# Performance work log

Hardware: AMD Instinct MI355X
Metric: run time of the kernel (lower is better)

## Reference

```python
import jax, jax.numpy as jnp
import numpy as np

B, S = 32, 256          # batch, sequence
D = 128                 # d_model
I = 256                 # mamba intermediate = 2*D
N = 16                  # ssm state size
R = 8                   # dt rank = ceil(D/16)
K = 4                   # conv kernel
L = 4                   # num mamba layers
Z = 128                 # vib z_dim
FUT = 20                # future steps


def setup_inputs() -> dict:
    key = jax.random.key(0)
    ks = iter(jax.random.split(key, 40))

    def nrm(shape, scale=0.02):
        return jax.random.normal(next(ks), shape, dtype=jnp.float32) * scale

    return {
        "x_cam": jax.random.normal(next(ks), (B, S, 8, 1024), dtype=jnp.float32),
        "x_ego": jax.random.normal(next(ks), (B, S, 64), dtype=jnp.float32),
        "vib_eps": jax.random.normal(next(ks), (B, Z), dtype=jnp.float32),
        "vis_w1": nrm((8 * 1024, 512)), "vis_b1": jnp.zeros((512,), jnp.float32),
        "vis_w2": nrm((512, D)), "vis_b2": jnp.zeros((D,), jnp.float32),
        "ego_w": nrm((64, D)), "ego_b": jnp.zeros((D,), jnp.float32),
        "fus_w": nrm((2 * D, D)), "fus_b": jnp.zeros((D,), jnp.float32),
        "norm_w": jnp.ones((L, D), jnp.float32),
        "in_proj_w": nrm((L, D, 2 * I)),
        "conv_w": nrm((L, I, K), 0.1), "conv_b": jnp.zeros((L, I), jnp.float32),
        "x_proj_w": nrm((L, I, R + 2 * N)),
        "dt_proj_w": nrm((L, R, I), 0.1), "dt_proj_b": jnp.full((L, I), -2.0, jnp.float32),
        "A_log": jnp.tile(jnp.log(jnp.arange(1, N + 1, dtype=jnp.float32))[None, None, :], (L, I, 1)),
        "D_par": jnp.ones((L, I), jnp.float32),
        "out_proj_w": nrm((L, I, D)),
        "normf_w": jnp.ones((D,), jnp.float32),
        "mu_w": nrm((D, Z)), "mu_b": jnp.zeros((Z,), jnp.float32),
        "lv_w": nrm((D, Z)), "lv_b": jnp.zeros((Z,), jnp.float32),
        "h1_w": nrm((Z, 256)), "h1_b": jnp.zeros((256,), jnp.float32),
        "h2_w": nrm((256, FUT * 2)), "h2_b": jnp.zeros((FUT * 2,), jnp.float32),
    }


def _rms(x, w, eps=1e-5):
    return x * jax.lax.rsqrt(jnp.mean(x * x, axis=-1, keepdims=True) + eps) * w


def _mixer(x, inw, cw, cb, xpw, dtw, dtb, alog, dpar, outw):
    # x: [B,S,D]
    Bb, Ss, _ = x.shape
    h, gate = jnp.split(x @ inw, 2, axis=-1)            # [B,S,I] each
    # depthwise causal conv (kernel K)
    hp = jnp.pad(h, ((0, 0), (K - 1, 0), (0, 0)))
    h = sum(hp[:, k:k + Ss, :] * cw[:, k] for k in range(K)) + cb
    h = jax.nn.silu(h)
    ssm = h @ xpw                                        # [B,S,R+2N]
    dt = jax.nn.softplus(ssm[..., :R] @ dtw + dtb)       # [B,S,I]
    Bm = ssm[..., R:R + N]                               # [B,S,N]
    Cm = ssm[..., R + N:]                                # [B,S,N]
    A = -jnp.exp(alog)                                   # [I,N]
    dA = jnp.exp(dt[..., None] * A)                      # [B,S,I,N]
    dBu = dt[..., None] * Bm[:, :, None, :] * h[..., None]  # [B,S,I,N]

    def step(carry, t):
        dA_t, dBu_t, C_t = t
        carry = carry * dA_t + dBu_t                     # [B,I,N]
        return carry, jnp.einsum('bin,bn->bi', carry, C_t)

    h0 = jnp.zeros((Bb, I, N), dtype=x.dtype)
    _, ys = jax.lax.scan(step, h0, (dA.swapaxes(0, 1), dBu.swapaxes(0, 1), Cm.swapaxes(0, 1)))
    y = ys.swapaxes(0, 1) + h * dpar                     # [B,S,I]
    y = y * jax.nn.silu(gate)
    return y @ outw                                      # [B,S,D]


def _mamba(x, norm_w, in_proj_w, conv_w, conv_b, x_proj_w, dt_proj_w, dt_proj_b, A_log, D_par, out_proj_w, normf_w):
    for l in range(L):
        x = x + _mixer(_rms(x, norm_w[l]), in_proj_w[l], conv_w[l], conv_b[l],
                       x_proj_w[l], dt_proj_w[l], dt_proj_b[l], A_log[l], D_par[l], out_proj_w[l])
    return _rms(x, normf_w)


def _forward(x_cam, x_ego, vib_eps, vis_w1, vis_b1, vis_w2, vis_b2, ego_w, ego_b, fus_w, fus_b,
             norm_w, in_proj_w, conv_w, conv_b, x_proj_w, dt_proj_w, dt_proj_b, A_log, D_par,
             out_proj_w, normf_w, mu_w, mu_b, lv_w, lv_b, h1_w, h1_b, h2_w, h2_b):
    Bb, Ss = x_cam.shape[:2]
    v = x_cam.reshape(Bb, Ss, -1)                                          # [B,S,8192]
    v = jax.nn.gelu(v @ vis_w1 + vis_b1, approximate=False) @ vis_w2 + vis_b2
    e = x_ego @ ego_w + ego_b
    fused = jax.nn.gelu(jnp.concatenate([v, e], axis=-1) @ fus_w + fus_b, approximate=False)
    h = _mamba(fused, norm_w, in_proj_w, conv_w, conv_b, x_proj_w,
               dt_proj_w, dt_proj_b, A_log, D_par, out_proj_w, normf_w)
    last = h[:, -1, :]                                                     # [B,D]
    mu = last @ mu_w + mu_b
    logvar = last @ lv_w + lv_b
    z = mu + vib_eps * jnp.exp(0.5 * logvar)
    kl = -0.5 * jnp.mean(1.0 + logvar - mu * mu - jnp.exp(logvar))
    out = jax.nn.relu(z @ h1_w + h1_b) @ h2_w + h2_b
    return out.reshape(Bb, FUT, 2), kl


def reference(x_cam, x_ego, vib_eps, vis_w1, vis_b1, vis_w2, vis_b2, ego_w, ego_b, fus_w, fus_b,
              norm_w, in_proj_w, conv_w, conv_b, x_proj_w, dt_proj_w, dt_proj_b, A_log, D_par,
              out_proj_w, normf_w, mu_w, mu_b, lv_w, lv_b, h1_w, h1_b, h2_w, h2_b):
    return _forward(x_cam, x_ego, vib_eps, vis_w1, vis_b1, vis_w2, vis_b2, ego_w, ego_b, fus_w, fus_b,
                    norm_w, in_proj_w, conv_w, conv_b, x_proj_w, dt_proj_w, dt_proj_b, A_log, D_par,
                    out_proj_w, normf_w, mu_w, mu_b, lv_w, lv_b, h1_w, h1_b, h2_w, h2_b)
```

## Files before the change

kernel.cpp:

```cpp
#include <hip/hip_runtime.h>
#include <hip/hip_bf16.h>
#include <math.h>

#define BQ 32
#define SQ 256
#define MTOK 8192
#define DD 128
#define II 256
#define NNs 16
#define RRs 8
#define KKs 4
#define LLs 4
#define ZZs 128
#define FUTs 20

typedef __attribute__((ext_vector_type(8))) short bf8v;
typedef __attribute__((ext_vector_type(4))) float f4v;

__device__ __forceinline__ float geluf(float x){ return 0.5f*x*(1.0f+erff(x*0.70710678118654752f)); }
__device__ __forceinline__ float siluf(float x){ return x/(1.0f+__expf(-x)); }
__device__ __forceinline__ float softplusf(float x){ return fmaxf(x,0.0f)+log1pf(__expf(-fabsf(x))); }
__device__ __forceinline__ unsigned short f2bf(float x){
    __hip_bfloat16 h = __float2bfloat16(x);
    return *reinterpret_cast<unsigned short*>(&h);
}

template<int ACT,int ADD,int OUTBF,typename AT>
__launch_bounds__(256,2)
__global__ void gemm_bf16_kernel(const AT* __restrict__ A,
                                 const unsigned short* __restrict__ Bt,
                                 const float* __restrict__ bias,
                                 void* __restrict__ Cv,
                                 int M, int N, int Kd, int ldc)
{
    constexpr int LDK = 72;
    __shared__ unsigned short As[128*LDK];
    __shared__ unsigned short Bs[64*LDK];
    const int tid = threadIdx.x;
    const int w = tid >> 6, lane = tid & 63;
    const int ml = lane & 15, quad = lane >> 4;
    const int rowBase = blockIdx.x * 128, colBase = blockIdx.y * 64;

    f4v acc[2][4];
    #pragma unroll
    for (int i=0;i<2;i++)
      #pragma unroll
      for (int j=0;j<4;j++) acc[i][j] = (f4v){0.f,0.f,0.f,0.f};

    bf8v pa[4], pb[2];
    const int ar = tid >> 3, as8 = (tid & 7) * 8;

    auto loadTile = [&](int kt){
        #pragma unroll
        for (int e=0;e<4;e++){
            int r = ar + e*32;
            if constexpr (sizeof(AT)==2){
                pa[e] = *reinterpret_cast<const bf8v*>(
                    (const unsigned short*)A + (size_t)(rowBase+r)*Kd + kt + as8);
            } else {
                const float* ap = (const float*)A + (size_t)(rowBase+r)*Kd + kt + as8;
                float4 v0 = *reinterpret_cast<const float4*>(ap);
                float4 v1 = *reinterpret_cast<const float4*>(ap+4);
                union { unsigned short u[8]; bf8v v; } o;
                o.u[0]=f2bf(v0.x); o.u[1]=f2bf(v0.y); o.u[2]=f2bf(v0.z); o.u[3]=f2bf(v0.w);
                o.u[4]=f2bf(v1.x); o.u[5]=f2bf(v1.y); o.u[6]=f2bf(v1.z); o.u[7]=f2bf(v1.w);
                pa[e] = o.v;
            }
        }
        #pragma unroll
        for (int e=0;e<2;e++){
            int r = ar + e*32;
            pb[e] = *reinterpret_cast<const bf8v*>(
                Bt + (size_t)(colBase+r)*Kd + kt + as8);
        }
    };

    loadTile(0);

    for (int kt=0; kt<Kd; kt+=64){
        #pragma unroll
        for (int e=0;e<4;e++) *reinterpret_cast<bf8v*>(&As[(ar+e*32)*LDK + as8]) = pa[e];
        #pragma unroll
        for (int e=0;e<2;e++) *reinterpret_cast<bf8v*>(&Bs[(ar+e*32)*LDK + as8]) = pb[e];
        __syncthreads();
        if (kt + 64 < Kd) loadTile(kt + 64);
        #pragma unroll
        for (int ks=0; ks<2; ks++){
            bf8v a0 = *reinterpret_cast<bf8v*>(&As[(w*32 +      ml)*LDK + ks*32 + quad*8]);
            bf8v a1 = *reinterpret_cast<bf8v*>(&As[(w*32 + 16 + ml)*LDK + ks*32 + quad*8]);
            #pragma unroll
            for (int nt=0; nt<4; nt++){
                bf8v b = *reinterpret_cast<bf8v*>(&Bs[(nt*16+ml)*LDK + ks*32 + quad*8]);
                acc[0][nt] = __builtin_amdgcn_mfma_f32_16x16x32_bf16(a0, b, acc[0][nt], 0,0,0);
                acc[1][nt] = __builtin_amdgcn_mfma_f32_16x16x32_bf16(a1, b, acc[1][nt], 0,0,0);
            }
        }
        __syncthreads();
    }

    #pragma unroll
    for (int mt=0; mt<2; mt++){
        #pragma unroll
        for (int nt=0; nt<4; nt++){
            int col = colBase + nt*16 + ml;
            float bb = bias ? bias[col] : 0.0f;
            #pragma unroll
            for (int r=0;r<4;r++){
                int row = rowBase + w*32 + mt*16 + quad*4 + r;
                float v = acc[mt][nt][r] + bb;
                if (ACT==1) v = geluf(v);
                if constexpr (OUTBF==1){
                    ((unsigned short*)Cv)[(size_t)row*ldc + col] = f2bf(v);
                } else {
                    float* cp = (float*)Cv + (size_t)row*ldc + col;
                    if (ADD) v += *cp;
                    *cp = v;
                }
            }
        }
    }
}

__launch_bounds__(256)
__global__ void castT_kernel(const float* __restrict__ in, unsigned short* __restrict__ out,
                             int Kd, int N)
{
    __shared__ float t[64][65];
    int k0 = blockIdx.y*64, n0 = blockIdx.x*64;
    int c = threadIdx.x & 63, r4 = threadIdx.x >> 6;
    #pragma unroll
    for (int it=0; it<16; it++){
        int row = it*4 + r4;
        t[row][c] = in[(size_t)(k0+row)*N + n0 + c];
    }
    __syncthreads();
    #pragma unroll
    for (int it=0; it<16; it++){
        int row = it*4 + r4;
        out[(size_t)(n0+row)*Kd + k0 + c] = f2bf(t[c][row]);
    }
}

__launch_bounds__(256)
__global__ void rms_bf_kernel(const float* __restrict__ x, const float* __restrict__ w,
                              unsigned short* __restrict__ out)
{
    int tid = threadIdx.x;
    int lane = tid & 63, wv = tid >> 6;
    int token = blockIdx.x*4 + wv;
    const float* xr = x + (size_t)token*DD;
    float v0 = xr[lane], v1 = xr[lane+64];
    float ss = v0*v0 + v1*v1;
    #pragma unroll
    for (int off=32; off>0; off>>=1) ss += __shfl_xor(ss, off);
    float r = rsqrtf(ss*(1.0f/DD) + 1e-5f);
    unsigned short* o = out + (size_t)token*DD;
    o[lane]    = f2bf(v0*r*w[lane]);
    o[lane+64] = f2bf(v1*r*w[lane+64]);
}

__launch_bounds__(256)
__global__ void conv_kernel(const float* __restrict__ hg, const float* __restrict__ cw,
                            const float* __restrict__ cb, float* __restrict__ hc)
{
    int idx = blockIdx.x*256 + threadIdx.x;
    int i = idx & (II-1);
    int m = idx >> 8;
    int s = m & (SQ-1);
    const float* w = cw + i*KKs;
    float a = cb[i];
    #pragma unroll
    for (int k=0;k<KKs;k++){
        int ssrc = s + k - (KKs-1);
        if (ssrc >= 0) a += hg[(size_t)(m + k - (KKs-1))*(2*II) + i] * w[k];
    }
    hc[idx] = siluf(a);
}

__launch_bounds__(64)
__global__ void xproj_dt_kernel(const float* __restrict__ hconv, const float* __restrict__ xpw,
                                const float* __restrict__ dtw, const float* __restrict__ dtbv,
                                float* __restrict__ dt_out, float* __restrict__ bc)
{
    __shared__ float hrow[II];
    __shared__ float ssm[RRs + 2*NNs];
    int m = blockIdx.x, tid = threadIdx.x;
    for (int t=tid; t<II; t+=64) hrow[t] = hconv[(size_t)m*II + t];
    __syncthreads();
    if (tid < 40){
        float a = 0.0f;
        #pragma unroll 8
        for (int k=0;k<II;k++) a += hrow[k]*xpw[k*40 + tid];
        ssm[tid] = a;
    }
    __syncthreads();
    if (tid < 32) bc[(size_t)m*32 + tid] = ssm[8 + tid];
    for (int ii=tid; ii<II; ii+=64){
        float a = dtbv[ii];
        #pragma unroll
        for (int r=0;r<RRs;r++) a += ssm[r]*dtw[r*II + ii];
        dt_out[(size_t)m*II + ii] = softplusf(a);
    }
}

__launch_bounds__(256)
__global__ void scan_kernel(const float* __restrict__ dtp, const float* __restrict__ bc,
                            const float* __restrict__ hconv, const float* __restrict__ hg,
                            const float* __restrict__ A_log, const float* __restrict__ D_par,
                            unsigned short* __restrict__ ybf)
{
    __shared__ float sdt[16][17], shv[16][17], sgv[16][17], sbc[16][33];
    int b = blockIdx.x >> 4, chunk = blockIdx.x & 15;
    int tid = threadIdx.x;
    int n = tid & 15, il = tid >> 4;
    int i = chunk*16 + il;
    float A2 = -__expf(A_log[i*NNs + n]) * 1.44269504f;
    float carry = 0.0f;
    const float dpi = D_par[i];
    const int m0 = b*SQ;
    const int li = tid & 15, ls = tid >> 4;
    const int gi = chunk*16 + li;
    for (int cs=0; cs<16; cs++){
        __syncthreads();
        int mload = m0 + cs*16 + ls;
        sdt[ls][li] = dtp[(size_t)mload*II + gi];
        shv[ls][li] = hconv[(size_t)mload*II + gi];
        sgv[ls][li] = hg[(size_t)mload*(2*II) + II + gi];
        sbc[ls][li]      = bc[(size_t)mload*32 + li];
        sbc[ls][li + 16] = bc[(size_t)mload*32 + 16 + li];
        __syncthreads();
        #pragma unroll
        for (int s=0; s<16; s++){
            float dtv = sdt[s][il];
            float hv  = shv[s][il];
            float dA  = exp2f(dtv*A2);
            carry = carry*dA + dtv*hv*sbc[s][n];
            float acc = carry*sbc[s][16+n];
            acc += __shfl_xor(acc, 1);
            acc += __shfl_xor(acc, 2);
            acc += __shfl_xor(acc, 4);
            acc += __shfl_xor(acc, 8);
            if (n == 0){
                ybf[(size_t)(m0 + cs*16 + s)*II + i] =
                    f2bf((acc + hv*dpi) * siluf(sgv[s][il]));
            }
        }
    }
}

__launch_bounds__(128)
__global__ void head_kernel(const float* __restrict__ x, const float* __restrict__ normf,
                            const float* __restrict__ mu_w, const float* __restrict__ mu_b,
                            const float* __restrict__ lv_w, const float* __restrict__ lv_b,
                            const float* __restrict__ eps, const float* __restrict__ h1_w,
                            const float* __restrict__ h1_b, const float* __restrict__ h2_w,
                            const float* __restrict__ h2_b, float* __restrict__ out,
                            float* __restrict__ klacc)
{
    __shared__ float lasts[DD];
    __shared__ float zs[DD];
    __shared__ float hr[256];
    __shared__ float red[2];
    int b = blockIdx.x, d = threadIdx.x;
    int lane = d & 63, wv = d >> 6;
    float xv = x[((size_t)(b*SQ + SQ-1))*DD + d];
    float ss = xv*xv;
    #pragma unroll
    for (int off=32; off>0; off>>=1) ss += __shfl_xor(ss, off);
    if (lane==0) red[wv] = ss;
    __syncthreads();
    float tot = red[0] + red[1];
    float last = xv * rsqrtf(tot*(1.0f/DD) + 1e-5f) * normf[d];
    lasts[d] = last;
    __syncthreads();
    float mu = mu_b[d], lv = lv_b[d];
    for (int j=0;j<DD;j++){
        float lj = lasts[j];
        mu += lj*mu_w[j*DD + d];
        lv += lj*lv_w[j*DD + d];
    }
    float z = mu + eps[b*ZZs + d]*__expf(0.5f*lv);
    zs[d] = z;
    float klp = 1.0f + lv - mu*mu - __expf(lv);
    #pragma unroll
    for (int off=32; off>0; off>>=1) klp += __shfl_xor(klp, off);
    if (lane==0) red[wv] = klp;
    __syncthreads();
    if (d==0) atomicAdd(klacc, red[0]+red[1]);
    for (int o=d; o<256; o+=128){
        float a = h1_b[o];
        for (int j=0;j<DD;j++) a += zs[j]*h1_w[j*256 + o];
        hr[o] = fmaxf(a, 0.0f);
    }
    __syncthreads();
    if (d < 40){
        float a = h2_b[d];
        for (int k=0;k<256;k++) a += hr[k]*h2_w[k*40 + d];
        out[b*(FUTs*2) + d] = a;
    }
}

__global__ void kl_final_kernel(const float* __restrict__ klacc, float* __restrict__ out)
{
    out[0] = -0.5f * klacc[0] * (1.0f/(BQ*ZZs));
}

extern "C" void kernel_launch(void* const* d_in, const int* in_sizes, int n_in,
                              void* d_out, int out_size, void* d_ws, size_t ws_size,
                              hipStream_t stream)
{
    const float* x_cam     = (const float*)d_in[0];
    const float* x_ego     = (const float*)d_in[1];
    const float* vib_eps   = (const float*)d_in[2];
    const float* vis_w1    = (const float*)d_in[3];
    const float* vis_b1    = (const float*)d_in[4];
    const float* vis_w2    = (const float*)d_in[5];
    const float* vis_b2    = (const float*)d_in[6];
    const float* ego_w     = (const float*)d_in[7];
    const float* ego_b     = (const float*)d_in[8];
    const float* fus_w     = (const float*)d_in[9];
    const float* fus_b     = (const float*)d_in[10];
    const float* norm_w    = (const float*)d_in[11];
    const float* in_proj_w = (const float*)d_in[12];
    const float* conv_w    = (const float*)d_in[13];
    const float* conv_b    = (const float*)d_in[14];
    const float* x_proj_w  = (const float*)d_in[15];
    const float* dt_proj_w = (const float*)d_in[16];
    const float* dt_proj_b = (const float*)d_in[17];
    const float* A_log     = (const float*)d_in[18];
    const float* D_par     = (const float*)d_in[19];
    const float* out_proj_w= (const float*)d_in[20];
    const float* normf_w   = (const float*)d_in[21];
    const float* mu_w      = (const float*)d_in[22];
    const float* mu_b      = (const float*)d_in[23];
    const float* lv_w      = (const float*)d_in[24];
    const float* lv_b      = (const float*)d_in[25];
    const float* h1_w      = (const float*)d_in[26];
    const float* h1_b      = (const float*)d_in[27];
    const float* h2_w      = (const float*)d_in[28];
    const float* h2_b      = (const float*)d_in[29];

    float* ws = (float*)d_ws;
    float* hg    = ws;
    unsigned short* v1g  = (unsigned short*)hg;
    float* hconv = ws + 4194304;
    unsigned short* catbf = (unsigned short*)hconv;
    float* xbuf  = ws + 6291456;
    float* dtws  = ws + 7340032;
    float* bcws  = ws + 9437184;
    unsigned short* ybf  = (unsigned short*)(ws + 9699328);
    unsigned short* xnbf = (unsigned short*)(ws + 10747904);
    unsigned short* w1t  = (unsigned short*)(ws + 11272192);
    unsigned short* w2t  = (unsigned short*)(ws + 13369344);
    unsigned short* egot = (unsigned short*)(ws + 13402112);
    unsigned short* fust = (unsigned short*)(ws + 13406208);
    unsigned short* wipt = (unsigned short*)(ws + 13422592);
    unsigned short* wopt = (unsigned short*)(ws + 13553664);
    float* klacc = ws + 13619200;

    hipMemsetAsync(klacc, 0, sizeof(float), stream);

    castT_kernel<<<dim3(8, 128), 256, 0, stream>>>(vis_w1, w1t, 8192, 512);
    castT_kernel<<<dim3(2, 8),   256, 0, stream>>>(vis_w2, w2t, 512, 128);
    castT_kernel<<<dim3(2, 1),   256, 0, stream>>>(ego_w,  egot, 64, 128);
    castT_kernel<<<dim3(2, 4),   256, 0, stream>>>(fus_w,  fust, 256, 128);
    for (int l=0; l<LLs; l++){
        castT_kernel<<<dim3(8, 2), 256, 0, stream>>>(
            in_proj_w + (size_t)l*DD*2*II, wipt + (size_t)l*2*II*DD, DD, 2*II);
        castT_kernel<<<dim3(2, 4), 256, 0, stream>>>(
            out_proj_w + (size_t)l*II*DD, wopt + (size_t)l*DD*II, II, DD);
    }

    gemm_bf16_kernel<1,0,1,float><<<dim3(64, 8), 256, 0, stream>>>(
        x_cam, w1t, vis_b1, v1g, MTOK, 512, 8192, 512);
    gemm_bf16_kernel<0,0,1,unsigned short><<<dim3(64, 2), 256, 0, stream>>>(
        v1g, w2t, vis_b2, catbf, MTOK, 128, 512, 256);
    gemm_bf16_kernel<0,0,1,float><<<dim3(64, 2), 256, 0, stream>>>(
        x_ego, egot, ego_b, catbf + 128, MTOK, 128, 64, 256);
    gemm_bf16_kernel<1,0,0,unsigned short><<<dim3(64, 2), 256, 0, stream>>>(
        catbf, fust, fus_b, xbuf, MTOK, 128, 256, 128);

    for (int l=0; l<LLs; l++){
        rms_bf_kernel<<<MTOK/4, 256, 0, stream>>>(xbuf, norm_w + l*DD, xnbf);
        gemm_bf16_kernel<0,0,0,unsigned short><<<dim3(64, 8), 256, 0, stream>>>(
            xnbf, wipt + (size_t)l*2*II*DD, nullptr, hg, MTOK, 2*II, DD, 2*II);
        conv_kernel<<<MTOK*II/256, 256, 0, stream>>>(
            hg, conv_w + (size_t)l*II*KKs, conv_b + (size_t)l*II, hconv);
        xproj_dt_kernel<<<MTOK, 64, 0, stream>>>(
            hconv, x_proj_w + (size_t)l*II*40, dt_proj_w + (size_t)l*RRs*II,
            dt_proj_b + (size_t)l*II, dtws, bcws);
        scan_kernel<<<BQ*16, 256, 0, stream>>>(
            dtws, bcws, hconv, hg, A_log + (size_t)l*II*NNs, D_par + (size_t)l*II, ybf);
        gemm_bf16_kernel<0,1,0,unsigned short><<<dim3(64, 2), 256, 0, stream>>>(
            ybf, wopt + (size_t)l*DD*II, nullptr, xbuf, MTOK, DD, II, DD);
    }

    head_kernel<<<BQ, 128, 0, stream>>>(
        xbuf, normf_w, mu_w, mu_b, lv_w, lv_b, vib_eps,
        h1_w, h1_b, h2_w, h2_b, (float*)d_out, klacc);
    kl_final_kernel<<<1, 1, 0, stream>>>(klacc, (float*)d_out + 1280);
}
```

Measured before the change: 1.195 ms.

## Use direct global-to-LDS double-buffered GEMM, pre-cast x_cam, batch xproj tokens

Adds a GEMM variant that stages A and B tiles with global_load_lds into double-buffered LDS, so the next tile streams in while MFMAs run and register staging goes away. When the workspace is large enough, x_cam is first cast to bf16 in a separate pass, so the big vision GEMM can use the new path. The xproj/dt kernel now handles 16 tokens per 256-thread block with vectorised LDS reads and dt weights kept in registers, replacing one 64-thread block per token. Risks: the extra cast pass writes and rereads a large bf16 copy of x_cam, and the unpadded LDS layout may cause bank conflicts.

Result: slower. 1.268 ms (+6.1%).

```diff
diff --git a/kernel.cpp b/kernel.cpp
--- a/kernel.cpp
+++ b/kernel.cpp
@@ -25,77 +25,68 @@
     return *reinterpret_cast<unsigned short*>(&h);
 }
 
-template<int ACT,int ADD,int OUTBF,typename AT>
+__device__ __forceinline__ void gload_lds16(const void* g, void* l){
+    __builtin_amdgcn_global_load_lds(
+        (const __attribute__((address_space(1))) void*)g,
+        (__attribute__((address_space(3))) void*)l, 16, 0, 0);
+}
+
+template<int ACT,int ADD,int OUTBF>
 __launch_bounds__(256,2)
-__global__ void gemm_bf16_kernel(const AT* __restrict__ A,
-                                 const unsigned short* __restrict__ Bt,
-                                 const float* __restrict__ bias,
-                                 void* __restrict__ Cv,
-                                 int M, int N, int Kd, int ldc)
-{
-    constexpr int LDK = 72;
-    __shared__ unsigned short As[128*LDK];
-    __shared__ unsigned short Bs[64*LDK];
+__global__ void gemm_lds_kernel(const unsigned short* __restrict__ A,
+                                const unsigned short* __restrict__ Bt,
+                                const float* __restrict__ bias,
+                                void* __restrict__ Cv,
+                                int M, int N, int Kd, int ldc)
+{
+    __shared__ unsigned short As[2][128*64];
+    __shared__ unsigned short Bs[2][64*64];
     const int tid = threadIdx.x;
     const int w = tid >> 6, lane = tid & 63;
     const int ml = lane & 15, quad = lane >> 4;
     const int rowBase = blockIdx.x * 128, colBase = blockIdx.y * 64;
 
+    const int srow = w*8 + (lane>>3);
+    const int scol = (lane&7)*8;
+
     f4v acc[2][4];
     #pragma unroll
     for (int i=0;i<2;i++)
       #pragma unroll
       for (int j=0;j<4;j++) acc[i][j] = (f4v){0.f,0.f,0.f,0.f};
 
-    bf8v pa[4], pb[2];
-    const int ar = tid >> 3, as8 = (tid & 7) * 8;
-
-    auto loadTile = [&](int kt){
+    auto stage = [&](int buf, int kt){
         #pragma unroll
         for (int e=0;e<4;e++){
-            int r = ar + e*32;
-            if constexpr (sizeof(AT)==2){
-                pa[e] = *reinterpret_cast<const bf8v*>(
-                    (const unsigned short*)A + (size_t)(rowBase+r)*Kd + kt + as8);
-            } else {
-                const float* ap = (const float*)A + (size_t)(rowBase+r)*Kd + kt + as8;
-                float4 v0 = *reinterpret_cast<const float4*>(ap);
-                float4 v1 = *reinterpret_cast<const float4*>(ap+4);
-                union { unsigned short u[8]; bf8v v; } o;
-                o.u[0]=f2bf(v0.x); o.u[1]=f2bf(v0.y); o.u[2]=f2bf(v0.z); o.u[3]=f2bf(v0.w);
-                o.u[4]=f2bf(v1.x); o.u[5]=f2bf(v1.y); o.u[6]=f2bf(v1.z); o.u[7]=f2bf(v1.w);
-                pa[e] = o.v;
-            }
+            const unsigned short* src = A + (size_t)(rowBase + srow + e*32)*Kd + kt + scol;
+            gload_lds16(src, (unsigned short*)As[buf] + (w + e*4)*512);
         }
         #pragma unroll
         for (int e=0;e<2;e++){
-            int r = ar + e*32;
-            pb[e] = *reinterpret_cast<const bf8v*>(
-                Bt + (size_t)(colBase+r)*Kd + kt + as8);
+            const unsigned short* src = Bt + (size_t)(colBase + srow + e*32)*Kd + kt + scol;
+            gload_lds16(src, (unsigned short*)Bs[buf] + (w + e*4)*512);
         }
     };
 
-    loadTile(0);
-
+    stage(0, 0);
+    __syncthreads();
+
+    int cur = 0;
     for (int kt=0; kt<Kd; kt+=64){
-        #pragma unroll
-        for (int e=0;e<4;e++) *reinterpret_cast<bf8v*>(&As[(ar+e*32)*LDK + as8]) = pa[e];
-        #pragma unroll
-        for (int e=0;e<2;e++) *reinterpret_cast<bf8v*>(&Bs[(ar+e*32)*LDK + as8]) = pb[e];
-        __syncthreads();
-        if (kt + 64 < Kd) loadTile(kt + 64);
+        if (kt + 64 < Kd) stage(cur^1, kt+64);
         #pragma unroll
         for (int ks=0; ks<2; ks++){
-            bf8v a0 = *reinterpret_cast<bf8v*>(&As[(w*32 +      ml)*LDK + ks*32 + quad*8]);
-            bf8v a1 = *reinterpret_cast<bf8v*>(&As[(w*32 + 16 + ml)*LDK + ks*32 + quad*8]);
+            bf8v a0 = *reinterpret_cast<const bf8v*>(&As[cur][(w*32 +      ml)*64 + ks*32 + quad*8]);
+            bf8v a1 = *reinterpret_cast<const bf8v*>(&As[cur][(w*32 + 16 + ml)*64 + ks*32 + quad*8]);
             #pragma unroll
             for (int nt=0; nt<4; nt++){
-                bf8v b = *reinterpret_cast<bf8v*>(&Bs[(nt*16+ml)*LDK + ks*32 + quad*8]);
+                bf8v b = *reinterpret_cast<const bf8v*>(&Bs[cur][(nt*16+ml)*64 + ks*32 + quad*8]);
                 acc[0][nt] = __builtin_amdgcn_mfma_f32_16x16x32_bf16(a0, b, acc[0][nt], 0,0,0);
                 acc[1][nt] = __builtin_amdgcn_mfma_f32_16x16x32_bf16(a1, b, acc[1][nt], 0,0,0);
             }
         }
         __syncthreads();
+        cur ^= 1;
     }
 
     #pragma unroll
@@ -121,6 +112,114 @@
     }
 }
 
+template<int ACT,int ADD,int OUTBF,typename AT>
+__launch_bounds__(256,2)
+__global__ void gemm_bf16_kernel(const AT* __restrict__ A,
+                                 const unsigned short* __restrict__ Bt,
+                                 const float* __restrict__ bias,
+                                 void* __restrict__ Cv,
+                                 int M, int N, int Kd, int ldc)
+{
+    constexpr int LDK = 72;
+    __shared__ unsigned short As[128*LDK];
+    __shared__ unsigned short Bs[64*LDK];
+    const int tid = threadIdx.x;
+    const int w = tid >> 6, lane = tid & 63;
+    const int ml = lane & 15, quad = lane >> 4;
+    const int rowBase = blockIdx.x * 128, colBase = blockIdx.y * 64;
+
+    f4v acc[2][4];
+    #pragma unroll
+    for (int i=0;i<2;i++)
+      #pragma unroll
+      for (int j=0;j<4;j++) acc[i][j] = (f4v){0.f,0.f,0.f,0.f};
+
+    bf8v pa[4], pb[2];
+    const int ar = tid >> 3, as8 = (tid & 7) * 8;
+
+    auto loadTile = [&](int kt){
+        #pragma unroll
+        for (int e=0;e<4;e++){
+            int r = ar + e*32;
+            if constexpr (sizeof(AT)==2){
+                pa[e] = *reinterpret_cast<const bf8v*>(
+                    (const unsigned short*)A + (size_t)(rowBase+r)*Kd + kt + as8);
+            } else {
+                const float* ap = (const float*)A + (size_t)(rowBase+r)*Kd + kt + as8;
+                float4 v0 = *reinterpret_cast<const float4*>(ap);
+                float4 v1 = *reinterpret_cast<const float4*>(ap+4);
+                union { unsigned short u[8]; bf8v v; } o;
+                o.u[0]=f2bf(v0.x); o.u[1]=f2bf(v0.y); o.u[2]=f2bf(v0.z); o.u[3]=f2bf(v0.w);
+                o.u[4]=f2bf(v1.x); o.u[5]=f2bf(v1.y); o.u[6]=f2bf(v1.z); o.u[7]=f2bf(v1.w);
+                pa[e] = o.v;
+            }
+        }
+        #pragma unroll
+        for (int e=0;e<2;e++){
+            int r = ar + e*32;
+            pb[e] = *reinterpret_cast<const bf8v*>(
+                Bt + (size_t)(colBase+r)*Kd + kt + as8);
+        }
+    };
+
+    loadTile(0);
+
+    for (int kt=0; kt<Kd; kt+=64){
+        #pragma unroll
+        for (int e=0;e<4;e++) *reinterpret_cast<bf8v*>(&As[(ar+e*32)*LDK + as8]) = pa[e];
+        #pragma unroll
+        for (int e=0;e<2;e++) *reinterpret_cast<bf8v*>(&Bs[(ar+e*32)*LDK + as8]) = pb[e];
+        __syncthreads();
+        if (kt + 64 < Kd) loadTile(kt + 64);
+        #pragma unroll
+        for (int ks=0; ks<2; ks++){
+            bf8v a0 = *reinterpret_cast<bf8v*>(&As[(w*32 +      ml)*LDK + ks*32 + quad*8]);
+            bf8v a1 = *reinterpret_cast<bf8v*>(&As[(w*32 + 16 + ml)*LDK + ks*32 + quad*8]);
+            #pragma unroll
+            for (int nt=0; nt<4; nt++){
+                bf8v b = *reinterpret_cast<bf8v*>(&Bs[(nt*16+ml)*LDK + ks*32 + quad*8]);
+                acc[0][nt] = __builtin_amdgcn_mfma_f32_16x16x32_bf16(a0, b, acc[0][nt], 0,0,0);
+                acc[1][nt] = __builtin_amdgcn_mfma_f32_16x16x32_bf16(a1, b, acc[1][nt], 0,0,0);
+            }
+        }
+        __syncthreads();
+    }
+
+    #pragma unroll
+    for (int mt=0; mt<2; mt++){
+        #pragma unroll
+        for (int nt=0; nt<4; nt++){
+            int col = colBase + nt*16 + ml;
+            float bb = bias ? bias[col] : 0.0f;
+            #pragma unroll
+            for (int r=0;r<4;r++){
+                int row = rowBase + w*32 + mt*16 + quad*4 + r;
+                float v = acc[mt][nt][r] + bb;
+                if (ACT==1) v = geluf(v);
+                if constexpr (OUTBF==1){
+                    ((unsigned short*)Cv)[(size_t)row*ldc + col] = f2bf(v);
+                } else {
+                    float* cp = (float*)Cv + (size_t)row*ldc + col;
+                    if (ADD) v += *cp;
+                    *cp = v;
+                }
+            }
+        }
+    }
+}
+
+__launch_bounds__(256)
+__global__ void cast_bf16_kernel(const float* __restrict__ in, unsigned short* __restrict__ out)
+{
+    size_t i = (size_t)blockIdx.x*256 + threadIdx.x;
+    const float4 v0 = reinterpret_cast<const float4*>(in)[i*2];
+    const float4 v1 = reinterpret_cast<const float4*>(in)[i*2+1];
+    union { unsigned short u[8]; bf8v v; } o;
+    o.u[0]=f2bf(v0.x); o.u[1]=f2bf(v0.y); o.u[2]=f2bf(v0.z); o.u[3]=f2bf(v0.w);
+    o.u[4]=f2bf(v1.x); o.u[5]=f2bf(v1.y); o.u[6]=f2bf(v1.z); o.u[7]=f2bf(v1.w);
+    reinterpret_cast<bf8v*>(out)[i] = o.v;
+}
+
 __launch_bounds__(256)
 __global__ void castT_kernel(const float* __restrict__ in, unsigned short* __restrict__ out,
                              int Kd, int N)
@@ -177,29 +276,65 @@
     hc[idx] = siluf(a);
 }
 
-__launch_bounds__(64)
-__global__ void xproj_dt_kernel(const float* __restrict__ hconv, const float* __restrict__ xpw,
-                                const float* __restrict__ dtw, const float* __restrict__ dtbv,
-                                float* __restrict__ dt_out, float* __restrict__ bc)
-{
-    __shared__ float hrow[II];
-    __shared__ float ssm[RRs + 2*NNs];
-    int m = blockIdx.x, tid = threadIdx.x;
-    for (int t=tid; t<II; t+=64) hrow[t] = hconv[(size_t)m*II + t];
-    __syncthreads();
-    if (tid < 40){
-        float a = 0.0f;
-        #pragma unroll 8
-        for (int k=0;k<II;k++) a += hrow[k]*xpw[k*40 + tid];
-        ssm[tid] = a;
-    }
-    __syncthreads();
-    if (tid < 32) bc[(size_t)m*32 + tid] = ssm[8 + tid];
-    for (int ii=tid; ii<II; ii+=64){
-        float a = dtbv[ii];
-        #pragma unroll
-        for (int r=0;r<RRs;r++) a += ssm[r]*dtw[r*II + ii];
-        dt_out[(size_t)m*II + ii] = softplusf(a);
+#define XT 16
+__launch_bounds__(256)
+__global__ void xproj_fused_kernel(const float* __restrict__ hconv,
+                                   const float* __restrict__ xpw,
+                                   const float* __restrict__ dtw,
+                                   const float* __restrict__ dtb,
+                                   float* __restrict__ dt_out,
+                                   float* __restrict__ bc)
+{
+    __shared__ float sh[XT][II+4];
+    __shared__ float ssm_s[XT][40];
+    const int tid = threadIdx.x;
+    const int m0 = blockIdx.x * XT;
+
+    {
+        const float4* src = reinterpret_cast<const float4*>(hconv + (size_t)m0*II);
+        #pragma unroll
+        for (int e=0;e<4;e++){
+            int idx = e*256 + tid;
+            int t = idx >> 6, c = idx & 63;
+            *reinterpret_cast<float4*>(&sh[t][c*4]) = src[idx];
+        }
+    }
+    __syncthreads();
+
+    for (int e = tid; e < XT*40; e += 256){
+        int t = e / 40, o = e - t*40;
+        float a0=0.f, a1=0.f, a2=0.f, a3=0.f;
+        #pragma unroll 16
+        for (int k=0;k<II;k+=4){
+            float4 h4 = *reinterpret_cast<const float4*>(&sh[t][k]);
+            a0 += h4.x*xpw[(k+0)*40+o];
+            a1 += h4.y*xpw[(k+1)*40+o];
+            a2 += h4.z*xpw[(k+2)*40+o];
+            a3 += h4.w*xpw[(k+3)*40+o];
+        }
+        ssm_s[t][o] = (a0+a1)+(a2+a3);
+    }
+    __syncthreads();
+
+    #pragma unroll
+    for (int e = tid; e < XT*32; e += 256){
+        int t = e >> 5, n = e & 31;
+        bc[(size_t)(m0+t)*32 + n] = ssm_s[t][8+n];
+    }
+
+    {
+        const int i = tid;
+        float wr[RRs];
+        #pragma unroll
+        for (int r=0;r<RRs;r++) wr[r] = dtw[r*II + i];
+        const float bb = dtb[i];
+        #pragma unroll 4
+        for (int t=0;t<XT;t++){
+            float a = bb;
+            #pragma unroll
+            for (int r=0;r<RRs;r++) a += ssm_s[t][r]*wr[r];
+            dt_out[(size_t)(m0+t)*II + i] = softplusf(a);
+        }
     }
 }
 
@@ -357,6 +492,9 @@
     unsigned short* wipt = (unsigned short*)(ws + 13422592);
     unsigned short* wopt = (unsigned short*)(ws + 13553664);
     float* klacc = ws + 13619200;
+    unsigned short* xcbf = (unsigned short*)(ws + 13619208);
+    const size_t need_bytes = (size_t)(13619208 + 33554432) * 4;
+    const bool big_ws = (ws_size >= need_bytes);
 
     hipMemsetAsync(klacc, 0, sizeof(float), stream);
 
@@ -371,27 +509,33 @@
             out_proj_w + (size_t)l*II*DD, wopt + (size_t)l*DD*II, II, DD);
     }
 
-    gemm_bf16_kernel<1,0,1,float><<<dim3(64, 8), 256, 0, stream>>>(
-        x_cam, w1t, vis_b1, v1g, MTOK, 512, 8192, 512);
-    gemm_bf16_kernel<0,0,1,unsigned short><<<dim3(64, 2), 256, 0, stream>>>(
+    if (big_ws){
+        cast_bf16_kernel<<<32768, 256, 0, stream>>>(x_cam, xcbf);
+        gemm_lds_kernel<1,0,1><<<dim3(64, 8), 256, 0, stream>>>(
+            xcbf, w1t, vis_b1, v1g, MTOK, 512, 8192, 512);
+    } else {
+        gemm_bf16_kernel<1,0,1,float><<<dim3(64, 8), 256, 0, stream>>>(
+            x_cam, w1t, vis_b1, v1g, MTOK, 512, 8192, 512);
+    }
+    gemm_lds_kernel<0,0,1><<<dim3(64, 2), 256, 0, stream>>>(
         v1g, w2t, vis_b2, catbf, MTOK, 128, 512, 256);
     gemm_bf16_kernel<0,0,1,float><<<dim3(64, 2), 256, 0, stream>>>(
         x_ego, egot, ego_b, catbf + 128, MTOK, 128, 64, 256);
-    gemm_bf16_kernel<1,0,0,unsigned short><<<dim3(64, 2), 256, 0, stream>>>(
+    gemm_lds_kernel<1,0,0><<<dim3(64, 2), 256, 0, stream>>>(
         catbf, fust, fus_b, xbuf, MTOK, 128, 256, 128);
 
     for (int l=0; l<LLs; l++){
         rms_bf_kernel<<<MTOK/4, 256, 0, stream>>>(xbuf, norm_w + l*DD, xnbf);
-        gemm_bf16_kernel<0,0,0,unsigned short><<<dim3(64, 8), 256, 0, stream>>>(
+        gemm_lds_kernel<0,0,0><<<dim3(64, 8), 256, 0, stream>>>(
             xnbf, wipt + (size_t)l*2*II*DD, nullptr, hg, MTOK, 2*II, DD, 2*II);
         conv_kernel<<<MTOK*II/256, 256, 0, stream>>>(
             hg, conv_w + (size_t)l*II*KKs, conv_b + (size_t)l*II, hconv);
-        xproj_dt_kernel<<<MTOK, 64, 0, stream>>>(
+        xproj_fused_kernel<<<MTOK/XT, 256, 0, stream>>>(
             hconv, x_proj_w + (size_t)l*II*40, dt_proj_w + (size_t)l*RRs*II,
             dt_proj_b + (size_t)l*II, dtws, bcws);
         scan_kernel<<<BQ*16, 256, 0, stream>>>(
             dtws, bcws, hconv, hg, A_log + (size_t)l*II*NNs, D_par + (size_t)l*II, ybf);
-        gemm_bf16_kernel<0,1,0,unsigned short><<<dim3(64, 2), 256, 0, stream>>>(
+        gemm_lds_kernel<0,1,0><<<dim3(64, 2), 256, 0, stream>>>(
             ybf, wopt + (size_t)l*DD*II, nullptr, xbuf, MTOK, DD, II, DD);
     }
 
```
